# Optimization experiments

Hardware: AMD Instinct MI355X
Metric: run time of the kernel (lower is better)

## Reference

```python
import jax, jax.numpy as jnp
import numpy as np

N_NODES = 10000
N_EDGES = 320000
MUL = 32            # multiplicity of each input/output irrep
RADIAL = 8          # edge scalar (radial basis) dim
HID = 64            # fc_neurons widths
NUM_NEIGHBORS = 32.0
MIX = np.pi / 8.0
INV_SQRT2 = 1.0 / np.sqrt(2.0)   # per-path alpha: 2 paths feed each mid irrep
INV_SQRT3 = 1.0 / np.sqrt(3.0)   # w3j(1,1,0) normalization


def setup_inputs() -> dict:
    key = jax.random.key(0)
    ks = jax.random.split(key, 16)
    inp = {
        "node_input": jax.random.normal(ks[0], (N_NODES, 4 * MUL), jnp.float32),  # 32x0e+32x1o flat
        "edge_attr": jax.random.normal(ks[1], (N_EDGES, 4), jnp.float32),          # 1x0e+1x1o (sh l=0,1)
        "edge_scalar_attr": jax.random.uniform(ks[2], (N_EDGES, RADIAL), jnp.float32),
        # first linear: 32x0e+32x1o -> (32x0e+32x1o) + (32x0e+32x1o); columns [:MUL]=conv path, [MUL:]=self path
        "W1_0e": jax.random.normal(ks[3], (MUL, 2 * MUL), jnp.float32),
        "W1_1o": jax.random.normal(ks[4], (MUL, 2 * MUL), jnp.float32),
        # radial MLP
        "W_mlp1": jax.random.normal(ks[5], (RADIAL, HID), jnp.float32),
        "W_mlp2": jax.random.normal(ks[6], (HID, HID), jnp.float32),
        # per-instruction 'uvu' path weights (mul_v = 1 squeezed): shape (HID, MUL)
        "Wp_00": jax.random.normal(ks[7], (HID, MUL), jnp.float32),  # 0e x 0e -> 0e
        "Wp_01": jax.random.normal(ks[8], (HID, MUL), jnp.float32),  # 0e x 1o -> 1o
        "Wp_10": jax.random.normal(ks[9], (HID, MUL), jnp.float32),  # 1o x 0e -> 1o
        "Wp_11": jax.random.normal(ks[10], (HID, MUL), jnp.float32), # 1o x 1o -> 0e
        # final linear: 64x0e+64x1o -> 32x0e+32x1o
        "W2_0e": jax.random.normal(ks[11], (2 * MUL, MUL), jnp.float32),
        "W2_1o": jax.random.normal(ks[12], (2 * MUL, MUL), jnp.float32),
        "edge_src": jax.random.randint(ks[13], (N_EDGES,), 0, N_NODES, jnp.int32),
        "edge_dst": jax.random.randint(ks[14], (N_EDGES,), 0, N_NODES, jnp.int32),
    }
    return inp


def _forward(node_input, edge_attr, edge_scalar_attr,
             W1_0e, W1_1o, W_mlp1, W_mlp2,
             Wp_00, Wp_01, Wp_10, Wp_11, W2_0e, W2_1o,
             edge_src, edge_dst):
    N = node_input.shape[0]
    # split flat node features into irrep blocks: 32x0e (N,32), 32x1o (N,32,3)
    x0 = node_input[:, :MUL]
    x1 = node_input[:, MUL:].reshape(N, MUL, 3)

    # ---- equivariant Linear: input -> input + output (fan-in normalized) ----
    f0 = (x0 @ W1_0e) / np.sqrt(MUL)                           # (N, 2*MUL)
    f1 = jnp.einsum('nui,uw->nwi', x1, W1_1o) / np.sqrt(MUL)   # (N, 2*MUL, 3)
    feat0, self0 = f0[:, :MUL], f0[:, MUL:]
    feat1, self1 = f1[:, :MUL], f1[:, MUL:]

    # ---- gather to edges ----
    e0 = feat0[edge_src]        # (E, MUL)
    e1 = feat1[edge_src]        # (E, MUL, 3)
    ea0 = edge_attr[:, :1]      # (E, 1) 0e
    ea1 = edge_attr[:, 1:4]     # (E, 3) 1o

    # ---- radial MLP -> per-edge per-path weights ----
    h = jax.nn.gelu((edge_scalar_attr @ W_mlp1) / np.sqrt(RADIAL))
    h = jax.nn.gelu((h @ W_mlp2) / np.sqrt(HID))               # (E, HID)
    w00 = h @ Wp_00   # (E, MUL)
    w01 = h @ Wp_01
    w10 = h @ Wp_10
    w11 = h @ Wp_11

    # ---- CG tensor product, 'uvu' mode (mul_v = 1) ----
    out0_a = w00 * e0 * ea0                                   # 0e x 0e -> 0e   (E, MUL)
    out0_b = w11 * jnp.sum(e1 * ea1[:, None, :], -1) * INV_SQRT3  # 1o.1o -> 0e
    out1_a = (w01 * e0)[:, :, None] * ea1[:, None, :]         # 0e x 1o -> 1o   (E, MUL, 3)
    out1_b = (w10[:, :, None] * e1) * ea0[:, :, None]         # 1o x 0e -> 1o
    mid0 = jnp.concatenate([out0_a, out0_b], axis=1) * INV_SQRT2  # (E, 2*MUL)   64x0e
    mid1 = jnp.concatenate([out1_a, out1_b], axis=1) * INV_SQRT2  # (E, 2*MUL, 3) 64x1o

    # ---- scatter-add to destination nodes ----
    n0 = jax.ops.segment_sum(mid0, edge_dst, num_segments=N) / np.sqrt(NUM_NEIGHBORS)
    n1 = jax.ops.segment_sum(mid1, edge_dst, num_segments=N) / np.sqrt(NUM_NEIGHBORS)

    # ---- final equivariant Linear: 64x0e+64x1o -> 32x0e+32x1o ----
    conv0 = (n0 @ W2_0e) / np.sqrt(2 * MUL)                    # (N, MUL)
    conv1 = jnp.einsum('nui,uw->nwi', n1, W2_1o) / np.sqrt(2 * MUL)  # (N, MUL, 3)

    c, s = np.cos(MIX), np.sin(MIX)
    y0 = c * self0 + s * conv0
    y1 = c * self1 + s * conv1
    return jnp.concatenate([y0, y1.reshape(N, MUL * 3)], axis=1)  # (N, 128)


def reference(node_input, edge_attr, edge_scalar_attr,
              W1_0e, W1_1o, W_mlp1, W_mlp2,
              Wp_00, Wp_01, Wp_10, Wp_11, W2_0e, W2_1o,
              edge_src, edge_dst):
    return _forward(node_input, edge_attr, edge_scalar_attr,
                    W1_0e, W1_1o, W_mlp1, W_mlp2,
                    Wp_00, Wp_01, Wp_10, Wp_11, W2_0e, W2_1o,
                    edge_src, edge_dst)
```

## Files before the change

kernel.cpp:

```cpp
#include <hip/hip_runtime.h>

typedef unsigned int uint32;
typedef unsigned short ushrt;
typedef __attribute__((ext_vector_type(4))) float f32x4;
typedef __attribute__((ext_vector_type(2))) float f32x2;
typedef __attribute__((ext_vector_type(8))) _Float16 halfx8;
typedef __attribute__((ext_vector_type(4))) uint32 uint32x4;

#define N_NODES 10000
#define N_EDGES 320000

#define SC_W1      0.17677669529663687f
#define SC_MLP1    0.35355339059327373f
#define SC_MLP2    0.125f
#define INV_SQRT3  0.5773502691896258f
#define COS_MIX    0.9238795325112867f
#define SIN_CONV   0.04783542904563623f

#define WS_FEATP 0
#define I_CNT    1280000
#define I_OFF    1290016
#define U_REC    1300032
#define U_WF     2580032
#define U_WBUF   2587200

__device__ __forceinline__ uint32 packh2(float a, float b) {
    _Float16 ha = (_Float16)a, hb = (_Float16)b;
    return (uint32)__builtin_bit_cast(unsigned short, ha) |
           ((uint32)__builtin_bit_cast(unsigned short, hb) << 16);
}
__device__ __forceinline__ unsigned short h16(float x) {
    _Float16 h = (_Float16)x;
    return __builtin_bit_cast(unsigned short, h);
}
__device__ __forceinline__ unsigned short pack_fp8_2(float a, float b) {
    return (unsigned short)(__builtin_amdgcn_cvt_pk_fp8_f32(a, b, 0, false) & 0xffff);
}
__device__ __forceinline__ float gelu_fast(float x) {
    float x2 = x * x;
    float z = x * __builtin_fmaf(0.03567740814f, x2, 0.7978845608f);
    float E = __builtin_amdgcn_exp2f(z * -2.885390082f);
    return x * __builtin_amdgcn_rcpf(1.0f + E);
}

#define K1_CNT_BLOCKS  1250
#define K1_PREP_BLOCKS 7
__global__ __launch_bounds__(256) void k1_fused(
        const int* __restrict__ edge_dst, int* __restrict__ cnt,
        const float* __restrict__ Wm1, const float* __restrict__ Wm2,
        const float* __restrict__ Wp00, const float* __restrict__ Wp01,
        const float* __restrict__ Wp10, const float* __restrict__ Wp11,
        uint32* __restrict__ wf) {
    int b = blockIdx.x;
    if (b < K1_CNT_BLOCKS) {
        int e = b * 256 + threadIdx.x;
        atomicAdd(&cnt[edge_dst[e]], 1);
    } else {
        int gid = (b - K1_CNT_BLOCKS) * 256 + threadIdx.x;
        int f = gid >> 6, lane = gid & 63;
        int kq = (lane >> 4) * 8;
        int c15 = lane & 15;
        float vals[8];
        if (f < 4) {
            int c = 16 * f + c15;
#pragma unroll
            for (int j = 0; j < 8; ++j) { int k = kq + j; vals[j] = (k < 8) ? Wm1[k * 64 + c] : 0.f; }
        } else if (f < 12) {
            int idx = f - 4, nt = idx >> 1, ks = idx & 1;
            int c = 16 * nt + c15;
#pragma unroll
            for (int j = 0; j < 8; ++j) { int k = 32 * ks + kq + j; vals[j] = Wm2[k * 64 + c]; }
        } else {
            int idx = f - 12, nt = idx >> 1, ks = idx & 1;
            int c = 16 * nt + c15;
            int u = c & 31, m = c >> 5;
            const float* W = (m == 0) ? Wp00 : (m == 1) ? Wp01 : (m == 2) ? Wp10 : Wp11;
            float sc = (m == 3) ? 0.125f * INV_SQRT3 : 0.125f;
#pragma unroll
            for (int j = 0; j < 8; ++j) { int k = 32 * ks + kq + j; vals[j] = W[k * 32 + u] * sc; }
        }
        uint32* o = wf + f * 256 + lane * 4;
#pragma unroll
        for (int w = 0; w < 4; ++w) o[w] = packh2(vals[2 * w], vals[2 * w + 1]);
    }
}

__global__ __launch_bounds__(1024) void csr_scan(const int* __restrict__ cnt,
                                                 int* __restrict__ off) {
    __shared__ int partial[1024];
    int t = threadIdx.x;
    const int CHUNK = 10;
    int base = t * CHUNK;
    int s = 0;
#pragma unroll
    for (int j = 0; j < CHUNK; ++j) {
        int idx = base + j;
        s += (idx < N_NODES) ? cnt[idx] : 0;
    }
    partial[t] = s;
    __syncthreads();
    for (int o = 1; o < 1024; o <<= 1) {
        int v = partial[t];
        int add = (t >= o) ? partial[t - o] : 0;
        __syncthreads();
        partial[t] = v + add;
        __syncthreads();
    }
    int run = (t > 0) ? partial[t - 1] : 0;
    for (int j = 0; j < CHUNK; ++j) {
        int idx = base + j;
        if (idx < N_NODES) {
            off[idx] = run;
            run += cnt[idx];
        }
    }
    if (t == 1023) off[N_NODES] = run;
}

#define MLP_BLOCKS 1250
#define K3_NODE_BLOCKS 2500
__global__ __launch_bounds__(256) void k3_fused(
        const float* __restrict__ edge_scalar, const float* __restrict__ edge_attr,
        const int* __restrict__ src_in, const int* __restrict__ dst_in,
        int* __restrict__ off,
        const uint32* __restrict__ wf,
        uint32* __restrict__ wbuf, uint4* __restrict__ rec,
        const float* __restrict__ x,
        const float* __restrict__ W1_0e, const float* __restrict__ W1_1o,
        float* __restrict__ featp, float* __restrict__ out) {
    __shared__ unsigned short sh[4][1024];
    __shared__ uint32 ob[4][512];
    __shared__ float eaxs[4][16];
    __shared__ int   poss[4][16];
    __shared__ float xrow[4][128];

    int lane = threadIdx.x & 63;
    int wvq = threadIdx.x >> 6;

    if (blockIdx.x >= MLP_BLOCKS) {
        int node = (blockIdx.x - MLP_BLOCKS) * 4 + wvq;
        float2 v = *(const float2*)(x + (size_t)node * 128 + lane * 2);
        xrow[wvq][lane * 2]     = v.x;
        xrow[wvq][lane * 2 + 1] = v.y;
        __syncthreads();
        const float* sx = xrow[wvq];
        int w = lane;
        float f0 = 0.f, f1x = 0.f, f1y = 0.f, f1z = 0.f;
#pragma unroll
        for (int u = 0; u < 32; ++u) {
            float w0 = W1_0e[u * 64 + w];
            float w1 = W1_1o[u * 64 + w];
            f0  += sx[u] * w0;
            f1x += sx[32 + u * 3 + 0] * w1;
            f1y += sx[32 + u * 3 + 1] * w1;
            f1z += sx[32 + u * 3 + 2] * w1;
        }
        f0 *= SC_W1; f1x *= SC_W1; f1y *= SC_W1; f1z *= SC_W1;
        if (w < 32) {
            featp[node * 128 + w]      = f0;
            featp[node * 128 + 32 + w] = f1x;
            featp[node * 128 + 64 + w] = f1y;
            featp[node * 128 + 96 + w] = f1z;
        } else {
            int ww = w - 32;
            out[node * 128 + ww] = COS_MIX * f0;
            out[node * 128 + 32 + ww * 3 + 0] = COS_MIX * f1x;
            out[node * 128 + 32 + ww * 3 + 1] = COS_MIX * f1y;
            out[node * 128 + 32 + ww * 3 + 2] = COS_MIX * f1z;
        }
        return;
    }

    int wave_id = blockIdx.x * 4 + wvq;
    int kq = (lane >> 4) * 8;
    int r15 = lane & 15;

    const uint32x4* wfp = (const uint32x4*)wf;
    halfx8 wb1[4], wb2[4][2], wbp[8][2];
#pragma unroll
    for (int nt = 0; nt < 4; ++nt)
        wb1[nt] = __builtin_bit_cast(halfx8, wfp[nt * 64 + lane]);
#pragma unroll
    for (int nt = 0; nt < 4; ++nt)
#pragma unroll
        for (int ks = 0; ks < 2; ++ks)
            wb2[nt][ks] = __builtin_bit_cast(halfx8, wfp[(4 + nt * 2 + ks) * 64 + lane]);
#pragma unroll
    for (int nt = 0; nt < 8; ++nt)
#pragma unroll
        for (int ks = 0; ks < 2; ++ks)
            wbp[nt][ks] = __builtin_bit_cast(halfx8, wfp[(12 + nt * 2 + ks) * 64 + lane]);

    const f32x4 z4 = {0.f, 0.f, 0.f, 0.f};
    unsigned short* shw = sh[wvq];
    uint32* obw = ob[wvq];
    unsigned short* obw16 = (unsigned short*)obw;

    for (int g = wave_id; g < N_EDGES / 16; g += MLP_BLOCKS * 4) {
        int e0 = g * 16;

        halfx8 a0 = (halfx8)0;
        if (lane < 16) {
            int e = e0 + lane;
            const float* esp = edge_scalar + (size_t)e * 8;
            float4 p = *(const float4*)esp;
            float4 q = *(const float4*)(esp + 4);
            float4 av = *(const float4*)(edge_attr + (size_t)e * 4);
            int dn = dst_in[e];
            int sn = src_in[e];
            int pos = atomicAdd(&off[dn], 1);
            poss[wvq][lane] = pos;
            eaxs[wvq][lane] = av.x;
            uint4 rv;
            rv.x = __float_as_uint(av.y);
            rv.y = __float_as_uint(av.z);
            rv.z = __float_as_uint(av.w);
            rv.w = (uint32)sn;
            rec[pos] = rv;
            a0[0] = (_Float16)p.x; a0[1] = (_Float16)p.y;
            a0[2] = (_Float16)p.z; a0[3] = (_Float16)p.w;
            a0[4] = (_Float16)q.x; a0[5] = (_Float16)q.y;
            a0[6] = (_Float16)q.z; a0[7] = (_Float16)q.w;
        }

        f32x4 acc1[4];
#pragma unroll
        for (int nt = 0; nt < 4; ++nt)
            acc1[nt] = __builtin_amdgcn_mfma_f32_16x16x32_f16(a0, wb1[nt], z4, 0, 0, 0);
#pragma unroll
        for (int nt = 0; nt < 4; ++nt)
#pragma unroll
            for (int i = 0; i < 4; ++i) {
                float gv = gelu_fast(acc1[nt][i] * SC_MLP1);
                int rr = (lane >> 4) * 4 + i;
                int ix = rr * 64 + 16 * nt + r15;
                shw[ix ^ ((rr & 7) << 3)] = h16(gv);
            }
        halfx8 a1[2];
#pragma unroll
        for (int ks = 0; ks < 2; ++ks) {
            int ix = r15 * 64 + 32 * ks + kq;
            a1[ks] = __builtin_bit_cast(halfx8,
                       *(const uint32x4*)&shw[ix ^ ((r15 & 7) << 3)]);
        }

        f32x4 acc2[4];
#pragma unroll
        for (int nt = 0; nt < 4; ++nt) {
            acc2[nt] = __builtin_amdgcn_mfma_f32_16x16x32_f16(a1[0], wb2[nt][0], z4, 0, 0, 0);
            acc2[nt] = __builtin_amdgcn_mfma_f32_16x16x32_f16(a1[1], wb2[nt][1], acc2[nt], 0, 0, 0);
        }
#pragma unroll
        for (int nt = 0; nt < 4; ++nt)
#pragma unroll
            for (int i = 0; i < 4; ++i) {
                float gv = gelu_fast(acc2[nt][i] * SC_MLP2);
                int rr = (lane >> 4) * 4 + i;
                int ix = rr * 64 + 16 * nt + r15;
                shw[ix ^ ((rr & 7) << 3)] = h16(gv);
            }
        halfx8 a2[2];
#pragma unroll
        for (int ks = 0; ks < 2; ++ks) {
            int ix = r15 * 64 + 32 * ks + kq;
            a2[ks] = __builtin_bit_cast(halfx8,
                       *(const uint32x4*)&shw[ix ^ ((r15 & 7) << 3)]);
        }

        f32x4 accp[8];
#pragma unroll
        for (int nt = 0; nt < 8; ++nt) {
            accp[nt] = __builtin_amdgcn_mfma_f32_16x16x32_f16(a2[0], wbp[nt][0], z4, 0, 0, 0);
            accp[nt] = __builtin_amdgcn_mfma_f32_16x16x32_f16(a2[1], wbp[nt][1], accp[nt], 0, 0, 0);
        }

#pragma unroll
        for (int i = 0; i < 4; ++i) {
            int rr = (lane >> 4) * 4 + i;
            float eax = eaxs[wvq][rr];
            unsigned short* orow = obw16 + rr * 64;
            orow[r15]      = pack_fp8_2(accp[0][i] * eax, accp[2][i]);
            orow[16 + r15] = pack_fp8_2(accp[1][i] * eax, accp[3][i]);
            orow[32 + r15] = pack_fp8_2(accp[4][i] * eax, accp[6][i]);
            orow[48 + r15] = pack_fp8_2(accp[5][i] * eax, accp[7][i]);
        }
#pragma unroll
        for (int pass = 0; pass < 2; ++pass) {
            int r = pass * 8 + (lane >> 3);
            int pos = poss[wvq][r];
            int c4 = (lane & 7) * 4;
            uint32x4 v = *(const uint32x4*)&obw[r * 32 + c4];
            *(uint32x4*)(wbuf + (size_t)pos * 32 + c4) = v;
        }
    }
}

__global__ __launch_bounds__(256) void gather(const int* __restrict__ off,
                                              const int* __restrict__ cnt,
                                              const uint4* __restrict__ rec,
                                              const uint32* __restrict__ wbuf,
                                              const float* __restrict__ featp,
                                              const float* __restrict__ W2_0e,
                                              const float* __restrict__ W2_1o,
                                              float* __restrict__ out) {
    int wv = threadIdx.x >> 6;
    int lane = threadIdx.x & 63;
    int node = blockIdx.x * 4 + wv;
    int u = lane & 31;
    int half = lane >> 5;

    int end = __builtin_amdgcn_readfirstlane(off[node]);
    int beg = end - __builtin_amdgcn_readfirstlane(cnt[node]);

    float a0acc = 0.f, a1x = 0.f, a1y = 0.f, a1z = 0.f;
    int offA = u + half * 32, offB = 64 + u, offC = 96 + u;
    const ushrt* wbuf16 = (const ushrt*)wbuf;
    int uslot = (half << 5) + u;

    for (int i0 = beg; i0 < end; i0 += 64) {
        int nn = end - i0;
        if (nn > 64) nn = 64;
        int idx = i0 + ((lane < nn) ? lane : 0);
        uint4 rv = rec[idx];
        int eyv = (int)rv.x, ezv = (int)rv.y, ewv = (int)rv.z, svv = (int)rv.w;
        for (int j0 = 0; j0 < nn; j0 += 4) {
            uint32 wl_[4];
            float fa_[4], fb_[4], fc_[4], ey_[4], ez_[4], ew_[4];
#pragma unroll
            for (int t = 0; t < 4; ++t) {
                int j = j0 + t;
                int jc = (j < nn) ? j : nn - 1;
                ey_[t] = __uint_as_float((uint32)__builtin_amdgcn_readlane(eyv, jc));
                ez_[t] = __uint_as_float((uint32)__builtin_amdgcn_readlane(ezv, jc));
                ew_[t] = __uint_as_float((uint32)__builtin_amdgcn_readlane(ewv, jc));
                int s  = __builtin_amdgcn_readlane(svv, jc);
                uint32 wl = (uint32)wbuf16[(size_t)(i0 + jc) * 64 + uslot];
                wl_[t] = (j < nn) ? wl : 0u;
                const float* fp = featp + (size_t)s * 128;
                fa_[t] = fp[offA];
                fb_[t] = fp[offB];
                fc_[t] = fp[offC];
            }
#pragma unroll
            for (int t = 0; t < 4; ++t) {
                f32x2 wab = __builtin_amdgcn_cvt_pk_f32_fp8((int)wl_[t], false);
                float wa = wab.x;
                float wb = wab.y;
                float va = half ? ey_[t] : 1.0f;
                float vb = half ? ez_[t] : 0.0f;
                float vc = half ? ew_[t] : 0.0f;
                float dot = fa_[t] * va + fb_[t] * vb + fc_[t] * vc;
                float w0s = half ? wb : wa;
                a0acc += w0s * dot;
                float m  = half ? wa : wb * fa_[t];
                float vx = half ? fa_[t] : ey_[t];
                float vy = half ? fb_[t] : ez_[t];
                float vz = half ? fc_[t] : ew_[t];
                a1x += m * vx; a1y += m * vy; a1z += m * vz;
            }
        }
    }

    __shared__ float red[4][256];
    float* r = red[wv];
    int c = (half << 5) + u;
    r[c] = a0acc;
    int b = 64 + c * 3;
    r[b] = a1x; r[b + 1] = a1y; r[b + 2] = a1z;
    __syncthreads();

    if (half == 0) {
        float acc = 0.f;
#pragma unroll 8
        for (int w = 0; w < 64; ++w) acc += r[w] * W2_0e[w * 32 + u];
        int o = node * 128 + u;
        out[o] = out[o] + SIN_CONV * acc;
    } else {
        float c0 = 0.f, c1 = 0.f, c2 = 0.f;
#pragma unroll 8
        for (int w = 0; w < 64; ++w) {
            float bw = W2_1o[w * 32 + u];
            c0 += r[64 + w * 3 + 0] * bw;
            c1 += r[64 + w * 3 + 1] * bw;
            c2 += r[64 + w * 3 + 2] * bw;
        }
        int o = node * 128 + 32 + u * 3;
        out[o + 0] = out[o + 0] + SIN_CONV * c0;
        out[o + 1] = out[o + 1] + SIN_CONV * c1;
        out[o + 2] = out[o + 2] + SIN_CONV * c2;
    }
}

extern "C" void kernel_launch(void* const* d_in, const int* in_sizes, int n_in,
                              void* d_out, int out_size, void* d_ws, size_t ws_size,
                              hipStream_t stream) {
    const float* node_input  = (const float*)d_in[0];
    const float* edge_attr   = (const float*)d_in[1];
    const float* edge_scalar = (const float*)d_in[2];
    const float* W1_0e       = (const float*)d_in[3];
    const float* W1_1o       = (const float*)d_in[4];
    const float* W_mlp1      = (const float*)d_in[5];
    const float* W_mlp2      = (const float*)d_in[6];
    const float* Wp00        = (const float*)d_in[7];
    const float* Wp01        = (const float*)d_in[8];
    const float* Wp10        = (const float*)d_in[9];
    const float* Wp11        = (const float*)d_in[10];
    const float* W2_0e       = (const float*)d_in[11];
    const float* W2_1o       = (const float*)d_in[12];
    const int*   edge_src    = (const int*)d_in[13];
    const int*   edge_dst    = (const int*)d_in[14];
    float* ws   = (float*)d_ws;
    int*   wsI  = (int*)d_ws;
    uint32* wsU = (uint32*)d_ws;
    uint4* recp = (uint4*)(wsU + U_REC);
    float* outp = (float*)d_out;

    hipMemsetAsync(wsI + I_CNT, 0, (N_NODES + 1) * sizeof(int), stream);

    k1_fused<<<K1_CNT_BLOCKS + K1_PREP_BLOCKS, 256, 0, stream>>>(
        edge_dst, wsI + I_CNT,
        W_mlp1, W_mlp2, Wp00, Wp01, Wp10, Wp11, wsU + U_WF);
    csr_scan<<<1, 1024, 0, stream>>>(wsI + I_CNT, wsI + I_OFF);
    k3_fused<<<MLP_BLOCKS + K3_NODE_BLOCKS, 256, 0, stream>>>(
        edge_scalar, edge_attr, edge_src, edge_dst, wsI + I_OFF,
        wsU + U_WF, wsU + U_WBUF, recp,
        node_input, W1_0e, W1_1o, ws + WS_FEATP, outp);
    gather<<<N_NODES / 4, 256, 0, stream>>>(wsI + I_OFF, wsI + I_CNT, recp,
                                            wsU + U_WBUF, ws + WS_FEATP,
                                            W2_0e, W2_1o, outp);
}
```

Measured before the change: 120.0 us.

## Stage MLP weights in LDS instead of registers and double MLP grid

Per-wave register-resident MFMA weight fragments (112 VGPRs of halfx8) are replaced by a block-shared LDS copy loaded once per block, and the output staging buffer now aliases the per-wave hidden-activation scratch. The aim is to cut register pressure so more waves fit per CU, and MLP_BLOCKS is doubled to fill that occupancy. The cost is an LDS read per weight fragment on every edge group, plus a 28 KB LDS load and a block barrier at the start of each block. Reusing the sh buffer as ob is only safe if the a2 reads finish before the fp8 writes, which holds within a single wave.

```diff
diff --git a/kernel.cpp b/kernel.cpp
--- a/kernel.cpp
+++ b/kernel.cpp
@@ -117,7 +117,7 @@
     if (t == 1023) off[N_NODES] = run;
 }
 
-#define MLP_BLOCKS 1250
+#define MLP_BLOCKS 2500
 #define K3_NODE_BLOCKS 2500
 __global__ __launch_bounds__(256) void k3_fused(
         const float* __restrict__ edge_scalar, const float* __restrict__ edge_attr,
@@ -128,8 +128,8 @@
         const float* __restrict__ x,
         const float* __restrict__ W1_0e, const float* __restrict__ W1_1o,
         float* __restrict__ featp, float* __restrict__ out) {
+    __shared__ uint32x4 wfl[28 * 64];
     __shared__ unsigned short sh[4][1024];
-    __shared__ uint32 ob[4][512];
     __shared__ float eaxs[4][16];
     __shared__ int   poss[4][16];
     __shared__ float xrow[4][128];
@@ -171,29 +171,19 @@
         return;
     }
 
+    {
+        const uint32x4* s = (const uint32x4*)wf;
+        for (int i = threadIdx.x; i < 28 * 64; i += 256) wfl[i] = s[i];
+    }
+    __syncthreads();
+
     int wave_id = blockIdx.x * 4 + wvq;
     int kq = (lane >> 4) * 8;
     int r15 = lane & 15;
 
-    const uint32x4* wfp = (const uint32x4*)wf;
-    halfx8 wb1[4], wb2[4][2], wbp[8][2];
-#pragma unroll
-    for (int nt = 0; nt < 4; ++nt)
-        wb1[nt] = __builtin_bit_cast(halfx8, wfp[nt * 64 + lane]);
-#pragma unroll
-    for (int nt = 0; nt < 4; ++nt)
-#pragma unroll
-        for (int ks = 0; ks < 2; ++ks)
-            wb2[nt][ks] = __builtin_bit_cast(halfx8, wfp[(4 + nt * 2 + ks) * 64 + lane]);
-#pragma unroll
-    for (int nt = 0; nt < 8; ++nt)
-#pragma unroll
-        for (int ks = 0; ks < 2; ++ks)
-            wbp[nt][ks] = __builtin_bit_cast(halfx8, wfp[(12 + nt * 2 + ks) * 64 + lane]);
-
     const f32x4 z4 = {0.f, 0.f, 0.f, 0.f};
     unsigned short* shw = sh[wvq];
-    uint32* obw = ob[wvq];
+    uint32* obw = (uint32*)shw;
     unsigned short* obw16 = (unsigned short*)obw;
 
     for (int g = wave_id; g < N_EDGES / 16; g += MLP_BLOCKS * 4) {
@@ -225,8 +215,10 @@
 
         f32x4 acc1[4];
 #pragma unroll
-        for (int nt = 0; nt < 4; ++nt)
-            acc1[nt] = __builtin_amdgcn_mfma_f32_16x16x32_f16(a0, wb1[nt], z4, 0, 0, 0);
+        for (int nt = 0; nt < 4; ++nt) {
+            halfx8 bb = __builtin_bit_cast(halfx8, wfl[nt * 64 + lane]);
+            acc1[nt] = __builtin_amdgcn_mfma_f32_16x16x32_f16(a0, bb, z4, 0, 0, 0);
+        }
 #pragma unroll
         for (int nt = 0; nt < 4; ++nt)
 #pragma unroll
@@ -247,8 +239,10 @@
         f32x4 acc2[4];
 #pragma unroll
         for (int nt = 0; nt < 4; ++nt) {
-            acc2[nt] = __builtin_amdgcn_mfma_f32_16x16x32_f16(a1[0], wb2[nt][0], z4, 0, 0, 0);
-            acc2[nt] = __builtin_amdgcn_mfma_f32_16x16x32_f16(a1[1], wb2[nt][1], acc2[nt], 0, 0, 0);
+            halfx8 b0 = __builtin_bit_cast(halfx8, wfl[(4 + nt * 2 + 0) * 64 + lane]);
+            halfx8 b1 = __builtin_bit_cast(halfx8, wfl[(4 + nt * 2 + 1) * 64 + lane]);
+            acc2[nt] = __builtin_amdgcn_mfma_f32_16x16x32_f16(a1[0], b0, z4, 0, 0, 0);
+            acc2[nt] = __builtin_amdgcn_mfma_f32_16x16x32_f16(a1[1], b1, acc2[nt], 0, 0, 0);
         }
 #pragma unroll
         for (int nt = 0; nt < 4; ++nt)
@@ -270,8 +264,10 @@
         f32x4 accp[8];
 #pragma unroll
         for (int nt = 0; nt < 8; ++nt) {
-            accp[nt] = __builtin_amdgcn_mfma_f32_16x16x32_f16(a2[0], wbp[nt][0], z4, 0, 0, 0);
-            accp[nt] = __builtin_amdgcn_mfma_f32_16x16x32_f16(a2[1], wbp[nt][1], accp[nt], 0, 0, 0);
+            halfx8 b0 = __builtin_bit_cast(halfx8, wfl[(12 + nt * 2 + 0) * 64 + lane]);
+            halfx8 b1 = __builtin_bit_cast(halfx8, wfl[(12 + nt * 2 + 1) * 64 + lane]);
+            accp[nt] = __builtin_amdgcn_mfma_f32_16x16x32_f16(a2[0], b0, z4, 0, 0, 0);
+            accp[nt] = __builtin_amdgcn_mfma_f32_16x16x32_f16(a2[1], b1, accp[nt], 0, 0, 0);
         }
 
 #pragma unroll
```

New measurement: 126.1 us. +5.0%, slower.

## Interleave two edge groups per wave and mix node blocks into MLP grid

Applied to the files above, without the earlier changes.

The edge-MLP loop now processes two independent 16-edge groups at a time, each with its own shared-memory staging buffers. Their loads, MFMAs and GELU stages are interleaved to expose more instruction-level parallelism and hide latency. The loop is fully unrolled into two fixed iterations covering four groups per wave, which hard-codes the edge count and grid size. Block scheduling is also changed so every third block does edge MLP work and the others do node linear work, interleaving the two kinds of block across the GPU. This raises register and LDS use, which may lower occupancy.

```diff
diff --git a/kernel.cpp b/kernel.cpp
--- a/kernel.cpp
+++ b/kernel.cpp
@@ -128,17 +128,18 @@
         const float* __restrict__ x,
         const float* __restrict__ W1_0e, const float* __restrict__ W1_1o,
         float* __restrict__ featp, float* __restrict__ out) {
-    __shared__ unsigned short sh[4][1024];
+    __shared__ unsigned short sh[4][2][1024];
     __shared__ uint32 ob[4][512];
-    __shared__ float eaxs[4][16];
-    __shared__ int   poss[4][16];
+    __shared__ float eaxs[4][2][16];
+    __shared__ int   poss[4][2][16];
     __shared__ float xrow[4][128];
 
     int lane = threadIdx.x & 63;
     int wvq = threadIdx.x >> 6;
-
-    if (blockIdx.x >= MLP_BLOCKS) {
-        int node = (blockIdx.x - MLP_BLOCKS) * 4 + wvq;
+    int rb = blockIdx.x;
+
+    if (rb % 3 != 0) {
+        int node = ((rb / 3) * 2 + (rb % 3) - 1) * 4 + wvq;
         float2 v = *(const float2*)(x + (size_t)node * 128 + lane * 2);
         xrow[wvq][lane * 2]     = v.x;
         xrow[wvq][lane * 2 + 1] = v.y;
@@ -171,7 +172,7 @@
         return;
     }
 
-    int wave_id = blockIdx.x * 4 + wvq;
+    int wave_id = (rb / 3) * 4 + wvq;
     int kq = (lane >> 4) * 8;
     int r15 = lane & 15;
 
@@ -192,16 +193,15 @@
             wbp[nt][ks] = __builtin_bit_cast(halfx8, wfp[(12 + nt * 2 + ks) * 64 + lane]);
 
     const f32x4 z4 = {0.f, 0.f, 0.f, 0.f};
-    unsigned short* shw = sh[wvq];
+    unsigned short* shA = sh[wvq][0];
+    unsigned short* shB = sh[wvq][1];
     uint32* obw = ob[wvq];
     unsigned short* obw16 = (unsigned short*)obw;
 
-    for (int g = wave_id; g < N_EDGES / 16; g += MLP_BLOCKS * 4) {
-        int e0 = g * 16;
-
-        halfx8 a0 = (halfx8)0;
+    auto loadg = [&](int g, int slot, halfx8& a0) {
+        a0 = (halfx8)0;
         if (lane < 16) {
-            int e = e0 + lane;
+            int e = g * 16 + lane;
             const float* esp = edge_scalar + (size_t)e * 8;
             float4 p = *(const float4*)esp;
             float4 q = *(const float4*)(esp + 4);
@@ -209,8 +209,8 @@
             int dn = dst_in[e];
             int sn = src_in[e];
             int pos = atomicAdd(&off[dn], 1);
-            poss[wvq][lane] = pos;
-            eaxs[wvq][lane] = av.x;
+            poss[wvq][slot][lane] = pos;
+            eaxs[wvq][slot][lane] = av.x;
             uint4 rv;
             rv.x = __float_as_uint(av.y);
             rv.y = __float_as_uint(av.z);
@@ -222,62 +222,37 @@
             a0[4] = (_Float16)q.x; a0[5] = (_Float16)q.y;
             a0[6] = (_Float16)q.z; a0[7] = (_Float16)q.w;
         }
-
-        f32x4 acc1[4];
+    };
+    auto gelu_store = [&](f32x4* acc, float sc, unsigned short* shw) {
 #pragma unroll
         for (int nt = 0; nt < 4; ++nt)
-            acc1[nt] = __builtin_amdgcn_mfma_f32_16x16x32_f16(a0, wb1[nt], z4, 0, 0, 0);
-#pragma unroll
-        for (int nt = 0; nt < 4; ++nt)
 #pragma unroll
             for (int i = 0; i < 4; ++i) {
-                float gv = gelu_fast(acc1[nt][i] * SC_MLP1);
+                float gv = gelu_fast(acc[nt][i] * sc);
                 int rr = (lane >> 4) * 4 + i;
                 int ix = rr * 64 + 16 * nt + r15;
                 shw[ix ^ ((rr & 7) << 3)] = h16(gv);
             }
-        halfx8 a1[2];
+    };
+    auto read_a = [&](unsigned short* shw, halfx8* a) {
 #pragma unroll
         for (int ks = 0; ks < 2; ++ks) {
             int ix = r15 * 64 + 32 * ks + kq;
-            a1[ks] = __builtin_bit_cast(halfx8,
-                       *(const uint32x4*)&shw[ix ^ ((r15 & 7) << 3)]);
-        }
-
-        f32x4 acc2[4];
-#pragma unroll
-        for (int nt = 0; nt < 4; ++nt) {
-            acc2[nt] = __builtin_amdgcn_mfma_f32_16x16x32_f16(a1[0], wb2[nt][0], z4, 0, 0, 0);
-            acc2[nt] = __builtin_amdgcn_mfma_f32_16x16x32_f16(a1[1], wb2[nt][1], acc2[nt], 0, 0, 0);
-        }
-#pragma unroll
-        for (int nt = 0; nt < 4; ++nt)
-#pragma unroll
-            for (int i = 0; i < 4; ++i) {
-                float gv = gelu_fast(acc2[nt][i] * SC_MLP2);
-                int rr = (lane >> 4) * 4 + i;
-                int ix = rr * 64 + 16 * nt + r15;
-                shw[ix ^ ((rr & 7) << 3)] = h16(gv);
-            }
-        halfx8 a2[2];
-#pragma unroll
-        for (int ks = 0; ks < 2; ++ks) {
-            int ix = r15 * 64 + 32 * ks + kq;
-            a2[ks] = __builtin_bit_cast(halfx8,
-                       *(const uint32x4*)&shw[ix ^ ((r15 & 7) << 3)]);
-        }
-
+            a[ks] = __builtin_bit_cast(halfx8,
+                      *(const uint32x4*)&shw[ix ^ ((r15 & 7) << 3)]);
+        }
+    };
+    auto proj_store = [&](halfx8* a2, int slot) {
         f32x4 accp[8];
 #pragma unroll
         for (int nt = 0; nt < 8; ++nt) {
             accp[nt] = __builtin_amdgcn_mfma_f32_16x16x32_f16(a2[0], wbp[nt][0], z4, 0, 0, 0);
             accp[nt] = __builtin_amdgcn_mfma_f32_16x16x32_f16(a2[1], wbp[nt][1], accp[nt], 0, 0, 0);
         }
-
 #pragma unroll
         for (int i = 0; i < 4; ++i) {
             int rr = (lane >> 4) * 4 + i;
-            float eax = eaxs[wvq][rr];
+            float eax = eaxs[wvq][slot][rr];
             unsigned short* orow = obw16 + rr * 64;
             orow[r15]      = pack_fp8_2(accp[0][i] * eax, accp[2][i]);
             orow[16 + r15] = pack_fp8_2(accp[1][i] * eax, accp[3][i]);
@@ -287,11 +262,56 @@
 #pragma unroll
         for (int pass = 0; pass < 2; ++pass) {
             int r = pass * 8 + (lane >> 3);
-            int pos = poss[wvq][r];
+            int pos = poss[wvq][slot][r];
             int c4 = (lane & 7) * 4;
             uint32x4 v = *(const uint32x4*)&obw[r * 32 + c4];
             *(uint32x4*)(wbuf + (size_t)pos * 32 + c4) = v;
         }
+    };
+
+#pragma unroll
+    for (int p = 0; p < 2; ++p) {
+        int gA = wave_id + p * 10000;
+        int gB = gA + 5000;
+
+        halfx8 a0A, a0B;
+        loadg(gA, 0, a0A);
+        loadg(gB, 1, a0B);
+
+        f32x4 acc1A[4], acc1B[4];
+#pragma unroll
+        for (int nt = 0; nt < 4; ++nt)
+            acc1A[nt] = __builtin_amdgcn_mfma_f32_16x16x32_f16(a0A, wb1[nt], z4, 0, 0, 0);
+#pragma unroll
+        for (int nt = 0; nt < 4; ++nt)
+            acc1B[nt] = __builtin_amdgcn_mfma_f32_16x16x32_f16(a0B, wb1[nt], z4, 0, 0, 0);
+        gelu_store(acc1A, SC_MLP1, shA);
+        gelu_store(acc1B, SC_MLP1, shB);
+
+        halfx8 a1A[2], a1B[2];
+        read_a(shA, a1A);
+        read_a(shB, a1B);
+
+        f32x4 acc2A[4], acc2B[4];
+#pragma unroll
+        for (int nt = 0; nt < 4; ++nt) {
+            acc2A[nt] = __builtin_amdgcn_mfma_f32_16x16x32_f16(a1A[0], wb2[nt][0], z4, 0, 0, 0);
+            acc2A[nt] = __builtin_amdgcn_mfma_f32_16x16x32_f16(a1A[1], wb2[nt][1], acc2A[nt], 0, 0, 0);
+        }
+#pragma unroll
+        for (int nt = 0; nt < 4; ++nt) {
+            acc2B[nt] = __builtin_amdgcn_mfma_f32_16x16x32_f16(a1B[0], wb2[nt][0], z4, 0, 0, 0);
+            acc2B[nt] = __builtin_amdgcn_mfma_f32_16x16x32_f16(a1B[1], wb2[nt][1], acc2B[nt], 0, 0, 0);
+        }
+        gelu_store(acc2A, SC_MLP2, shA);
+        gelu_store(acc2B, SC_MLP2, shB);
+
+        halfx8 a2A[2], a2B[2];
+        read_a(shA, a2A);
+        read_a(shB, a2B);
+
+        proj_store(a2A, 0);
+        proj_store(a2B, 1);
     }
 }
 
```

After: 123.5 us. 2.9% more time.
